# Optimization experiments

Hardware: AMD Instinct MI355X
Metric: run time of the kernel (lower is better)

Reference implementation:

```python
import jax, jax.numpy as jnp
import numpy as np

N = 100_000      # nodes
E = 400_000      # edges
POS = 3          # pos_dim
F = 128          # feats_dim (kernel_dim)
M = 16           # m_dim
FE = 16          # fourier_features
EIN = 2 * F + 2 * FE + 1   # 289 edge mlp input
EHID = 2 * EIN             # 578
NIN = F + M                # 144
NHID = 2 * F               # 256
EPS = 1e-5


def _ln(x, g, b):
    m = x.mean(-1, keepdims=True)
    v = ((x - m) ** 2).mean(-1, keepdims=True)
    return (x - m) * jax.lax.rsqrt(v + EPS) * g + b


def setup_inputs() -> dict:
    key = jax.random.key(0)
    ks = jax.random.split(key, 8)

    def xav(k, i, o):
        return jax.random.normal(k, (i, o), jnp.float32) * np.float32(np.sqrt(2.0 / (i + o)))

    x = jax.random.normal(ks[0], (N, POS + F), jnp.float32)
    edge_index = jax.random.randint(ks[1], (2, E), 0, N, dtype=jnp.int64)
    return {
        "x": x,
        "edge_index": edge_index,
        "e_w1": xav(ks[2], EIN, EHID), "e_b1": jnp.zeros((EHID,), jnp.float32),
        "e_w2": xav(ks[3], EHID, M),   "e_b2": jnp.zeros((M,), jnp.float32),
        "en1_g": jnp.ones((M,), jnp.float32), "en1_b": jnp.zeros((M,), jnp.float32),
        "en2_g": jnp.ones((M,), jnp.float32), "en2_b": jnp.zeros((M,), jnp.float32),
        "nn1_g": jnp.ones((F,), jnp.float32), "nn1_b": jnp.zeros((F,), jnp.float32),
        "n_w1": xav(ks[4], NIN, NHID), "n_b1": jnp.zeros((NHID,), jnp.float32),
        "n_w2": xav(ks[5], NHID, F),   "n_b2": jnp.zeros((F,), jnp.float32),
        "nn2_g": jnp.ones((F,), jnp.float32), "nn2_b": jnp.zeros((F,), jnp.float32),
    }


def reference(x, edge_index, e_w1, e_b1, e_w2, e_b2, en1_g, en1_b, en2_g, en2_b,
              nn1_g, nn1_b, n_w1, n_b1, n_w2, n_b2, nn2_g, nn2_b):
    coors, feats = x[:, :POS], x[:, POS:]
    src, dst = edge_index[0], edge_index[1]  # x_j = feats[src], x_i = feats[dst]

    rel = coors[src] - coors[dst]                      # [E,3]
    d = (rel ** 2).sum(-1, keepdims=True)              # [E,1] squared distance
    scales = jnp.asarray(2.0, jnp.float32) ** jnp.arange(FE)
    ds = d / scales                                    # [E,FE]
    edge_attr = jnp.concatenate([jnp.sin(ds), jnp.cos(ds), d], -1)  # [E,2*FE+1]

    # edge MLP + LayerNorm (message)
    m = jnp.concatenate([feats[dst], feats[src], edge_attr], -1)    # [E,EIN]
    m = jax.nn.silu(m @ e_w1 + e_b1)
    m = jax.nn.silu(m @ e_w2 + e_b2)                                # [E,M]
    m = _ln(m, en1_g, en1_b)

    # scatter-add to target nodes, then LayerNorm
    m_i = jax.ops.segment_sum(m, dst, num_segments=N)               # [N,M]
    m_i = _ln(m_i, en2_g, en2_b)

    # node update MLP with residual
    h = jnp.concatenate([_ln(feats, nn1_g, nn1_b), m_i], -1)        # [N,NIN]
    h = jax.nn.silu(h @ n_w1 + n_b1)
    h = h @ n_w2 + n_b2
    h = _ln(h, nn2_g, nn2_b)
    out = feats + h
    return jnp.concatenate([coors, out], -1)                        # [N,POS+F]
```

## Files before the change

### kernel.cpp

```cpp
#include <hip/hip_runtime.h>
#include <math.h>

#define N_NODES 100000
#define N_EDGES 400000
#define POSD 3
#define F 128
#define M 16
#define EIN 289
#define EHID 578
#define NIN 144
#define NHID 256
#define ROW 131
#define LNEPS 1e-5f

#define KP 320
#define NP 640
#define EPB 32
#define NSLICE 10
#define NTW 5
#define HIDP 640

#define NPB2 80
#define NK1 160
#define NK1P 168
#define NSL2 5
#define NHIDP 264

typedef _Float16 half8 __attribute__((ext_vector_type(8)));
typedef _Float16 half4 __attribute__((ext_vector_type(4)));
typedef float f32x4 __attribute__((ext_vector_type(4)));

__device__ __forceinline__ float silu_f(float v) { return v / (1.f + __expf(-v)); }

__global__ __launch_bounds__(256) void prep_feats(
    const float* __restrict__ x, _Float16* __restrict__ feats)
{
    long long i = (long long)blockIdx.x * 256 + threadIdx.x;
    if (i < (long long)N_NODES * F) {
        int n = (int)(i >> 7), k = (int)(i & 127);
        feats[i] = (_Float16)x[(long long)n * ROW + POSD + k];
    }
}

__global__ __launch_bounds__(256) void prep_weights(
    const float* __restrict__ w1, const float* __restrict__ w2,
    _Float16* __restrict__ w1ks, _Float16* __restrict__ w2t)
{
    long long idx = (long long)blockIdx.x * 256 + threadIdx.x;
    const long long n1 = (long long)NSLICE * NP * 32;
    if (idx < n1) {
        int s   = (int)(idx / (NP * 32));
        int rem = (int)(idx - (long long)s * (NP * 32));
        int c   = rem >> 5;
        int kk  = rem & 31;
        int k   = s * 32 + kk;
        float v = (k < EIN && c < EHID) ? w1[(long long)k * EHID + c] : 0.f;
        w1ks[idx] = (_Float16)v;
    } else {
        long long j = idx - n1;
        if (j < (long long)M * HIDP) {
            int oc = (int)(j / HIDP);
            int k  = (int)(j - (long long)oc * HIDP);
            float v = (k < EHID) ? w2[(long long)k * M + oc] : 0.f;
            w2t[j] = (_Float16)v;
        }
    }
}

__global__ __launch_bounds__(256) void prep_weights_node(
    const float* __restrict__ w1, const float* __restrict__ w2,
    _Float16* __restrict__ w1ks2, _Float16* __restrict__ w2ks)
{
    int idx = blockIdx.x * 256 + threadIdx.x;
    const int n1 = NSL2 * 256 * 32;
    if (idx < n1) {
        int s = idx >> 13, rem = idx & 8191;
        int c = rem >> 5, kk = rem & 31;
        int k = s * 32 + kk;
        w1ks2[idx] = (_Float16)((k < NIN) ? w1[k * NHID + c] : 0.f);
    } else if (idx < n1 + 8 * 128 * 32) {
        int j = idx - n1;
        int s = j >> 12, rem = j & 4095;
        int c = rem >> 5, kk = rem & 31;
        int k = s * 32 + kk;
        w2ks[j] = (_Float16)w2[k * F + c];
    }
}

__global__ __launch_bounds__(512, 4) void edge_kernel(
    const _Float16* __restrict__ feats, const float* __restrict__ x,
    const int* __restrict__ ei,
    const _Float16* __restrict__ w1ks, const float* __restrict__ b1,
    const _Float16* __restrict__ w2t, const float* __restrict__ b2,
    const float* __restrict__ g1, const float* __restrict__ bb1,
    float* __restrict__ m_i)
{
    __shared__ __align__(16) _Float16 smem[EPB * HIDP];
    _Float16* lds_A = smem;
    _Float16* lds_H = smem;
    __shared__ float part[4][EPB][M];
    __shared__ int   src_s[EPB], dst_s[EPB];
    __shared__ float d_s[EPB];

    const int t    = threadIdx.x;
    const int lane = t & 63;
    const int wv   = t >> 6;
    const int cl16 = lane & 15;
    const int h4   = lane >> 4;
    const long long ebase = (long long)blockIdx.x * EPB;

    if (t < EPB) {
        int s = ei[ebase + t];
        int d = ei[(long long)N_EDGES + ebase + t];
        src_s[t] = s; dst_s[t] = d;
        float dx = x[(long long)s*ROW+0] - x[(long long)d*ROW+0];
        float dy = x[(long long)s*ROW+1] - x[(long long)d*ROW+1];
        float dz = x[(long long)s*ROW+2] - x[(long long)d*ROW+2];
        d_s[t] = dx*dx + dy*dy + dz*dz;
    }
    __syncthreads();

    for (int i = t; i < EPB * 32; i += 512) {
        int row = i >> 5, g = i & 31;
        int node = (g < 16) ? dst_s[row] : src_s[row];
        half8 v = *(const half8*)(feats + (long long)node * F + ((g & 15) << 3));
        *(half8*)(lds_A + row * KP + ((g ^ (row & 7)) << 3)) = v;
    }
    for (int i = t; i < EPB * 64; i += 512) {
        int row = i >> 6, j = i & 63;
        float v;
        if (j < 16)       v = __sinf(ldexpf(d_s[row], -j));
        else if (j < 32)  v = __cosf(ldexpf(d_s[row], -(j - 16)));
        else if (j == 32) v = d_s[row];
        else              v = 0.f;
        int g = 32 + (j >> 3);
        lds_A[row * KP + ((g ^ (row & 7)) << 3) + (j & 7)] = (_Float16)v;
    }
    __syncthreads();

    f32x4 acc[2][NTW] = {};
    half8 bfA[NTW], bfB[NTW];
    {
        #pragma unroll
        for (int nt = 0; nt < NTW; ++nt) {
            int ntile = wv * NTW + nt;
            bfA[nt] = *(const half8*)(w1ks + ntile * 512 + cl16 * 32 + h4 * 8);
        }
    }
    #pragma unroll
    for (int s = 0; s < NSLICE; ++s) {
        if (s + 1 < NSLICE) {
            const _Float16* base = w1ks + (long long)(s + 1) * (NP * 32);
            #pragma unroll
            for (int nt = 0; nt < NTW; ++nt) {
                int ntile = wv * NTW + nt;
                half8 v = *(const half8*)(base + ntile * 512 + cl16 * 32 + h4 * 8);
                if (s & 1) bfA[nt] = v; else bfB[nt] = v;
            }
        }
        const int G = s * 4 + h4;
        const int aoff = ((G & ~7) | ((G ^ (cl16 & 7)) & 7)) << 3;
        half8 af[2];
        #pragma unroll
        for (int mt = 0; mt < 2; ++mt)
            af[mt] = *(const half8*)(lds_A + (mt * 16 + cl16) * KP + aoff);
        #pragma unroll
        for (int nt = 0; nt < NTW; ++nt) {
            half8 b = (s & 1) ? bfB[nt] : bfA[nt];
            #pragma unroll
            for (int mt = 0; mt < 2; ++mt)
                acc[mt][nt] = __builtin_amdgcn_mfma_f32_16x16x32_f16(
                                  af[mt], b, acc[mt][nt], 0, 0, 0);
        }
    }
    __syncthreads();

    #pragma unroll
    for (int nt = 0; nt < NTW; ++nt) {
        int hcol = (wv * NTW + nt) * 16 + cl16;
        float bias = (hcol < EHID) ? b1[hcol] : 0.f;
        int gcol = hcol >> 3;
        #pragma unroll
        for (int mt = 0; mt < 2; ++mt) {
            #pragma unroll
            for (int r = 0; r < 4; ++r) {
                int edge = mt * 16 + h4 * 4 + r;
                float v = (hcol < EHID) ? silu_f(acc[mt][nt][r] + bias) : 0.f;
                lds_H[edge * HIDP + (((gcol & ~7) | ((gcol ^ edge) & 7)) << 3) + (hcol & 7)]
                    = (_Float16)v;
            }
        }
    }
    __syncthreads();

    {
        const int eh = wv & 1;
        const int kq = wv >> 1;
        f32x4 acc2 = {};
        const int oc = cl16;
        const int edgeA = eh * 16 + oc;
        #pragma unroll
        for (int k5 = 0; k5 < 5; ++k5) {
            int ks = kq * 5 + k5;
            int G2 = ks * 4 + h4;
            const half8 a = *(const half8*)(lds_H + edgeA * HIDP +
                               (((G2 & ~7) | ((G2 ^ edgeA) & 7)) << 3));
            const half8 b = *(const half8*)(w2t + oc * HIDP + ks * 32 + h4 * 8);
            acc2 = __builtin_amdgcn_mfma_f32_16x16x32_f16(a, b, acc2, 0, 0, 0);
        }
        #pragma unroll
        for (int r = 0; r < 4; ++r)
            part[kq][eh * 16 + h4 * 4 + r][oc] = acc2[r];
    }
    __syncthreads();

    if (wv < 2) {
        const int eh = wv;
        const int oc = cl16;
        float g = g1[oc], bb = bb1[oc], b2v = b2[oc];
        #pragma unroll
        for (int r = 0; r < 4; ++r) {
            int edge = eh * 16 + h4 * 4 + r;
            float v = part[0][edge][oc] + part[1][edge][oc]
                    + part[2][edge][oc] + part[3][edge][oc] + b2v;
            v = silu_f(v);
            float s = v, s2 = v * v;
            #pragma unroll
            for (int m = 8; m >= 1; m >>= 1) {
                s  += __shfl_xor(s,  m, 16);
                s2 += __shfl_xor(s2, m, 16);
            }
            float mean = s * (1.f / 16.f);
            float var  = s2 * (1.f / 16.f) - mean * mean;
            float outv = (v - mean) * rsqrtf(var + LNEPS) * g + bb;
            atomicAdd(&m_i[(long long)dst_s[edge] * M + oc], outv);
        }
    }
}

__global__ __launch_bounds__(512, 4) void node_kernel(
    const _Float16* __restrict__ feats, const float* __restrict__ x,
    const float* __restrict__ m_i,
    const float* __restrict__ en2g, const float* __restrict__ en2b,
    const float* __restrict__ nn1g, const float* __restrict__ nn1b,
    const _Float16* __restrict__ w1ks2, const float* __restrict__ b1,
    const _Float16* __restrict__ w2ks, const float* __restrict__ b2,
    const float* __restrict__ nn2g, const float* __restrict__ nn2b,
    float* __restrict__ out)
{
    __shared__ __align__(16) _Float16 smem[NPB2 * NHIDP];
    _Float16* lds_A = smem;
    _Float16* lds_H = smem;
    __shared__ float rsum2[NPB2], rsq2[NPB2];

    const int t    = threadIdx.x;
    const int lane = t & 63;
    const int wv   = t >> 6;
    const int cl16 = lane & 15;
    const int h4   = lane >> 4;
    const long long nb = (long long)blockIdx.x * NPB2;

    if (t < NPB2) { rsum2[t] = 0.f; rsq2[t] = 0.f; }

    #pragma unroll
    for (int p = 0; p < 5; ++p) {
        int nl = p * 16 + (t >> 5);
        int l  = t & 31;
        half4 v4 = *(const half4*)(feats + (nb + nl) * F + l * 4);
        float v[4]; float s = 0.f, s2 = 0.f;
        #pragma unroll
        for (int i = 0; i < 4; ++i) {
            v[i] = (float)v4[i]; s += v[i]; s2 += v[i]*v[i];
        }
        #pragma unroll
        for (int m = 16; m >= 1; m >>= 1) {
            s  += __shfl_xor(s,  m, 32);
            s2 += __shfl_xor(s2, m, 32);
        }
        float mean = s * (1.f/128.f);
        float var  = s2 * (1.f/128.f) - mean*mean;
        float rs   = rsqrtf(var + LNEPS);
        half4 w;
        #pragma unroll
        for (int i = 0; i < 4; ++i) {
            int c = l * 4 + i;
            w[i] = (_Float16)((v[i] - mean) * rs * nn1g[c] + nn1b[c]);
        }
        *(half4*)(lds_A + nl * NK1P + l * 4) = w;
    }
    for (int i = t; i < NPB2 * M; i += 512) {
        int nl = i >> 4, oc = i & 15;
        float v = m_i[(nb + nl) * M + oc];
        float a = v, a2 = v * v;
        #pragma unroll
        for (int m = 8; m >= 1; m >>= 1) {
            a  += __shfl_xor(a,  m, 16);
            a2 += __shfl_xor(a2, m, 16);
        }
        float mn = a * (1.f/16.f);
        float vr = a2 * (1.f/16.f) - mn*mn;
        float lv = (v - mn) * rsqrtf(vr + LNEPS) * en2g[oc] + en2b[oc];
        lds_A[nl * NK1P + 128 + oc] = (_Float16)lv;
    }
    for (int i = t; i < NPB2 * 16; i += 512) {
        int nl = i >> 4, j = i & 15;
        lds_A[nl * NK1P + 144 + j] = (_Float16)0.f;
    }
    __syncthreads();

    f32x4 acc[5][2] = {};
    #pragma unroll
    for (int s = 0; s < NSL2; ++s) {
        half8 bf[2];
        #pragma unroll
        for (int nt = 0; nt < 2; ++nt) {
            int ntile = wv * 2 + nt;
            bf[nt] = *(const half8*)(w1ks2 + s * (NHID * 32)
                                     + ntile * 512 + cl16 * 32 + h4 * 8);
        }
        const int G = s * 4 + h4;
        half8 af[5];
        #pragma unroll
        for (int mt = 0; mt < 5; ++mt)
            af[mt] = *(const half8*)(lds_A + (mt * 16 + cl16) * NK1P + G * 8);
        #pragma unroll
        for (int nt = 0; nt < 2; ++nt) {
            #pragma unroll
            for (int mt = 0; mt < 5; ++mt)
                acc[mt][nt] = __builtin_amdgcn_mfma_f32_16x16x32_f16(
                                  af[mt], bf[nt], acc[mt][nt], 0, 0, 0);
        }
    }
    __syncthreads();

    #pragma unroll
    for (int nt = 0; nt < 2; ++nt) {
        int hcol = (wv * 2 + nt) * 16 + cl16;
        float bias = b1[hcol];
        #pragma unroll
        for (int mt = 0; mt < 5; ++mt) {
            #pragma unroll
            for (int r = 0; r < 4; ++r) {
                int row = mt * 16 + h4 * 4 + r;
                float v = silu_f(acc[mt][nt][r] + bias);
                lds_H[row * NHIDP + hcol] = (_Float16)v;
            }
        }
    }
    __syncthreads();

    f32x4 acc2[5] = {};
    const int col = wv * 16 + cl16;
    #pragma unroll
    for (int s = 0; s < 8; ++s) {
        const half8 b = *(const half8*)(w2ks + s * (F * 32) + col * 32 + h4 * 8);
        const int G2 = s * 4 + h4;
        #pragma unroll
        for (int mt = 0; mt < 5; ++mt) {
            int row = mt * 16 + cl16;
            const half8 a = *(const half8*)(lds_H + row * NHIDP + G2 * 8);
            acc2[mt] = __builtin_amdgcn_mfma_f32_16x16x32_f16(a, b, acc2[mt], 0, 0, 0);
        }
    }

    float y[5][4];
    float b2v = b2[col];
    #pragma unroll
    for (int mt = 0; mt < 5; ++mt) {
        #pragma unroll
        for (int r = 0; r < 4; ++r) {
            float v = acc2[mt][r] + b2v;
            y[mt][r] = v;
            float s = v, s2 = v * v;
            #pragma unroll
            for (int m = 8; m >= 1; m >>= 1) {
                s  += __shfl_xor(s,  m, 16);
                s2 += __shfl_xor(s2, m, 16);
            }
            if (cl16 == 0) {
                int row = mt * 16 + h4 * 4 + r;
                atomicAdd(&rsum2[row], s);
                atomicAdd(&rsq2[row],  s2);
            }
        }
    }
    __syncthreads();

    float gcol2 = nn2g[col], bcol2 = nn2b[col];
    #pragma unroll
    for (int mt = 0; mt < 5; ++mt) {
        #pragma unroll
        for (int r = 0; r < 4; ++r) {
            int row = mt * 16 + h4 * 4 + r;
            long long node = nb + row;
            float mn = rsum2[row] * (1.f/128.f);
            float vr = rsq2[row] * (1.f/128.f) - mn*mn;
            float rs = rsqrtf(vr + LNEPS);
            float res = x[node * ROW + POSD + col];
            out[node * ROW + POSD + col] = res + (y[mt][r] - mn) * rs * gcol2 + bcol2;
        }
    }
    for (int i = t; i < NPB2 * POSD; i += 512) {
        int nl = i / 3, c = i - nl * 3;
        long long node = nb + nl;
        out[node * ROW + c] = x[node * ROW + c];
    }
}

extern "C" void kernel_launch(void* const* d_in, const int* in_sizes, int n_in,
                              void* d_out, int out_size, void* d_ws, size_t ws_size,
                              hipStream_t stream) {
    const float* x    = (const float*)d_in[0];
    const int*   ei   = (const int*)d_in[1];
    const float* e_w1 = (const float*)d_in[2];
    const float* e_b1 = (const float*)d_in[3];
    const float* e_w2 = (const float*)d_in[4];
    const float* e_b2 = (const float*)d_in[5];
    const float* en1g = (const float*)d_in[6];
    const float* en1b = (const float*)d_in[7];
    const float* en2g = (const float*)d_in[8];
    const float* en2b = (const float*)d_in[9];
    const float* nn1g = (const float*)d_in[10];
    const float* nn1b = (const float*)d_in[11];
    const float* n_w1 = (const float*)d_in[12];
    const float* n_b1 = (const float*)d_in[13];
    const float* n_w2 = (const float*)d_in[14];
    const float* n_b2 = (const float*)d_in[15];
    const float* nn2g = (const float*)d_in[16];
    const float* nn2b = (const float*)d_in[17];
    float* out = (float*)d_out;

    char* ws = (char*)d_ws;
    float*    m_i   = (float*)ws;
    _Float16* w1ks  = (_Float16*)(ws + 6400000);
    _Float16* w2t   = (_Float16*)(ws + 6809600);
    _Float16* feats = (_Float16*)(ws + 6830080);
    _Float16* w1ks2 = (_Float16*)(ws + 32430080);
    _Float16* w2ks  = (_Float16*)(ws + 32512000);

    hipMemsetAsync(m_i, 0, (size_t)N_NODES * M * sizeof(float), stream);
    prep_weights<<<840, 256, 0, stream>>>(e_w1, e_w2, w1ks, w2t);
    prep_weights_node<<<288, 256, 0, stream>>>(n_w1, n_w2, w1ks2, w2ks);
    prep_feats<<<(N_NODES * F + 255) / 256, 256, 0, stream>>>(x, feats);
    edge_kernel<<<N_EDGES / EPB, 512, 0, stream>>>(
        feats, x, ei, w1ks, e_b1, w2t, e_b2, en1g, en1b, m_i);
    node_kernel<<<N_NODES / NPB2, 512, 0, stream>>>(
        feats, x, m_i, en2g, en2b, nn1g, nn1b, w1ks2, n_b1, w2ks, n_b2, nn2g, nn2b, out);
}
```

Before: 572.1 us.

## Replace XOR swizzle with padded LDS rows, skip dead tiles, prefetch w2 fragments

```diff
diff --git a/kernel.cpp b/kernel.cpp
--- a/kernel.cpp
+++ b/kernel.cpp
@@ -14,11 +14,13 @@
 #define LNEPS 1e-5f
 
 #define KP 320
+#define KPA 328
 #define NP 640
 #define EPB 32
 #define NSLICE 10
 #define NTW 5
 #define HIDP 640
+#define HIDPA 648
 
 #define NPB2 80
 #define NK1 160
@@ -95,7 +97,7 @@
     const float* __restrict__ g1, const float* __restrict__ bb1,
     float* __restrict__ m_i)
 {
-    __shared__ __align__(16) _Float16 smem[EPB * HIDP];
+    __shared__ __align__(16) _Float16 smem[EPB * HIDPA];
     _Float16* lds_A = smem;
     _Float16* lds_H = smem;
     __shared__ float part[4][EPB][M];
@@ -124,7 +126,7 @@
         int row = i >> 5, g = i & 31;
         int node = (g < 16) ? dst_s[row] : src_s[row];
         half8 v = *(const half8*)(feats + (long long)node * F + ((g & 15) << 3));
-        *(half8*)(lds_A + row * KP + ((g ^ (row & 7)) << 3)) = v;
+        *(half8*)(lds_A + row * KPA + (g << 3)) = v;
     }
     for (int i = t; i < EPB * 64; i += 512) {
         int row = i >> 6, j = i & 63;
@@ -133,44 +135,51 @@
         else if (j < 32)  v = __cosf(ldexpf(d_s[row], -(j - 16)));
         else if (j == 32) v = d_s[row];
         else              v = 0.f;
-        int g = 32 + (j >> 3);
-        lds_A[row * KP + ((g ^ (row & 7)) << 3) + (j & 7)] = (_Float16)v;
+        lds_A[row * KPA + 256 + j] = (_Float16)v;
     }
     __syncthreads();
 
     f32x4 acc[2][NTW] = {};
-    half8 bfA[NTW], bfB[NTW];
+    const bool live[NTW] = {
+        (wv * NTW + 0) * 16 < EHID, (wv * NTW + 1) * 16 < EHID,
+        (wv * NTW + 2) * 16 < EHID, (wv * NTW + 3) * 16 < EHID,
+        (wv * NTW + 4) * 16 < EHID };
+    #pragma unroll
+    for (int s = 0; s < NSLICE; ++s) {
+        half8 bf[NTW];
+        #pragma unroll
+        for (int nt = 0; nt < NTW; ++nt) {
+            if (live[nt]) {
+                int ntile = wv * NTW + nt;
+                bf[nt] = *(const half8*)(w1ks + (long long)s * (NP * 32)
+                                         + ntile * 512 + cl16 * 32 + h4 * 8);
+            }
+        }
+        const int G = s * 4 + h4;
+        half8 af[2];
+        #pragma unroll
+        for (int mt = 0; mt < 2; ++mt)
+            af[mt] = *(const half8*)(lds_A + (mt * 16 + cl16) * KPA + G * 8);
+        #pragma unroll
+        for (int nt = 0; nt < NTW; ++nt) {
+            if (live[nt]) {
+                #pragma unroll
+                for (int mt = 0; mt < 2; ++mt)
+                    acc[mt][nt] = __builtin_amdgcn_mfma_f32_16x16x32_f16(
+                                      af[mt], bf[nt], acc[mt][nt], 0, 0, 0);
+            }
+        }
+    }
+
+    half8 bq[5];
     {
-        #pragma unroll
-        for (int nt = 0; nt < NTW; ++nt) {
-            int ntile = wv * NTW + nt;
-            bfA[nt] = *(const half8*)(w1ks + ntile * 512 + cl16 * 32 + h4 * 8);
-        }
-    }
-    #pragma unroll
-    for (int s = 0; s < NSLICE; ++s) {
-        if (s + 1 < NSLICE) {
-            const _Float16* base = w1ks + (long long)(s + 1) * (NP * 32);
-            #pragma unroll
-            for (int nt = 0; nt < NTW; ++nt) {
-                int ntile = wv * NTW + nt;
-                half8 v = *(const half8*)(base + ntile * 512 + cl16 * 32 + h4 * 8);
-                if (s & 1) bfA[nt] = v; else bfB[nt] = v;
-            }
-        }
-        const int G = s * 4 + h4;
-        const int aoff = ((G & ~7) | ((G ^ (cl16 & 7)) & 7)) << 3;
-        half8 af[2];
-        #pragma unroll
-        for (int mt = 0; mt < 2; ++mt)
-            af[mt] = *(const half8*)(lds_A + (mt * 16 + cl16) * KP + aoff);
-        #pragma unroll
-        for (int nt = 0; nt < NTW; ++nt) {
-            half8 b = (s & 1) ? bfB[nt] : bfA[nt];
-            #pragma unroll
-            for (int mt = 0; mt < 2; ++mt)
-                acc[mt][nt] = __builtin_amdgcn_mfma_f32_16x16x32_f16(
-                                  af[mt], b, acc[mt][nt], 0, 0, 0);
+        const int eh = wv & 1;  (void)eh;
+        const int kq = wv >> 1;
+        const int oc = cl16;
+        #pragma unroll
+        for (int k5 = 0; k5 < 5; ++k5) {
+            int ks = kq * 5 + k5;
+            bq[k5] = *(const half8*)(w2t + oc * HIDP + ks * 32 + h4 * 8);
         }
     }
     __syncthreads();
@@ -179,15 +188,13 @@
     for (int nt = 0; nt < NTW; ++nt) {
         int hcol = (wv * NTW + nt) * 16 + cl16;
         float bias = (hcol < EHID) ? b1[hcol] : 0.f;
-        int gcol = hcol >> 3;
         #pragma unroll
         for (int mt = 0; mt < 2; ++mt) {
             #pragma unroll
             for (int r = 0; r < 4; ++r) {
                 int edge = mt * 16 + h4 * 4 + r;
                 float v = (hcol < EHID) ? silu_f(acc[mt][nt][r] + bias) : 0.f;
-                lds_H[edge * HIDP + (((gcol & ~7) | ((gcol ^ edge) & 7)) << 3) + (hcol & 7)]
-                    = (_Float16)v;
+                lds_H[edge * HIDPA + hcol] = (_Float16)v;
             }
         }
     }
@@ -203,10 +210,8 @@
         for (int k5 = 0; k5 < 5; ++k5) {
             int ks = kq * 5 + k5;
             int G2 = ks * 4 + h4;
-            const half8 a = *(const half8*)(lds_H + edgeA * HIDP +
-                               (((G2 & ~7) | ((G2 ^ edgeA) & 7)) << 3));
-            const half8 b = *(const half8*)(w2t + oc * HIDP + ks * 32 + h4 * 8);
-            acc2 = __builtin_amdgcn_mfma_f32_16x16x32_f16(a, b, acc2, 0, 0, 0);
+            const half8 a = *(const half8*)(lds_H + edgeA * HIDPA + G2 * 8);
+            acc2 = __builtin_amdgcn_mfma_f32_16x16x32_f16(a, bq[k5], acc2, 0, 0, 0);
         }
         #pragma unroll
         for (int r = 0; r < 4; ++r)
```

Result: faster. 512.4 us (-10.4%).
